# Performance work log

Measured on AMD Instinct MI355X. Metric: run time of the kernel, lower is better.

Reference implementation:

```python
import jax, jax.numpy as jnp
import numpy as np
from jax import lax

C = 256          # hidden_channels
K_ITERS = 3      # num_iterations

def _conv(x, w, b, stride=1, pad='SAME'):
    y = lax.conv_general_dilated(x, w, (stride, stride), pad,
                                 dimension_numbers=('NCHW', 'OIHW', 'NCHW'))
    return y + b[None, :, None, None]

def setup_inputs() -> dict:
    key = jax.random.key(0)
    ks = jax.random.split(key, 16)
    B, N, H, W = 1, 3, 384, 384
    def p(k, sh, scale=None):
        if scale is None:
            scale = 1.0 / np.sqrt(np.prod(sh[1:]))
        return jax.random.normal(k, sh, jnp.float32) * scale
    z = lambda: jnp.zeros((C,), jnp.float32)
    return {
        'frames': jax.random.normal(ks[0], (B, N, 3, H, W), jnp.float32),
        'backbone_w': p(ks[1], (C, 3, 8, 8)), 'backbone_b': z(),
        'W_intra': p(ks[2], (C, C), scale=1.0 / C),
        'W_inter': p(ks[3], (C, C), scale=1.0 / C),
        'gate_w': p(ks[4], (C, C, 1, 1)), 'gate_b': z(),
        'Wz': p(ks[5], (C, 2 * C, 3, 3)), 'bz': z(),
        'Wr': p(ks[6], (C, 2 * C, 3, 3)), 'br': z(),
        'Wh': p(ks[7], (C, 2 * C, 3, 3)), 'bh': z(),
        'ro_w1': p(ks[8], (C, 2 * C, 3, 3)), 'ro_b1': z(),
        'ro_w2': p(ks[9], (1, C, 3, 3)), 'ro_b2': jnp.zeros((1,), jnp.float32),
    }

def _forward(frames, backbone_w, backbone_b, W_intra, W_inter, gate_w, gate_b,
             Wz, bz, Wr, br, Wh, bh, ro_w1, ro_b1, ro_w2, ro_b2):
    B, N, _, H, W = frames.shape
    x = frames.reshape(B * N, 3, H, W)
    # backbone: stride-8 conv + ReLU -> node embeddings v (B*N, C, Hf, Wf)
    v = jax.nn.relu(_conv(x, backbone_w, backbone_b, stride=8, pad='VALID'))
    Hf, Wf = v.shape[2], v.shape[3]
    P = Hf * Wf
    v = v.reshape(B, N, C, Hf, Wf)
    h = v
    idx = jnp.arange(N)
    for _ in range(K_ITERS):
        hp = h.reshape(B, N, C, P).transpose(0, 1, 3, 2)      # (B,N,P,C)
        # inter attention e_ij = h_i W h_j^T over all ordered pairs
        t = jnp.einsum('bipc,cd->bipd', hp, W_inter)
        e = jnp.einsum('bipd,bjqd->bijpq', t, hp)              # (B,N,N,P,P)
        # intra (loop-edge) attention on the diagonal, own weight
        ti = jnp.einsum('bipc,cd->bipd', hp, W_intra)
        e_intra = jnp.einsum('bipd,biqd->bipq', ti, hp)        # (B,N,P,P)
        e = e.at[:, idx, idx].set(e_intra)
        attn = jax.nn.softmax(e, axis=-1)
        m = jnp.einsum('bijpq,bjqc->bijpc', attn, hp)          # msg j->i (B,N,N,P,C)
        m = m.transpose(0, 1, 2, 4, 3).reshape(B * N * N, C, Hf, Wf)
        # gated aggregation: sigmoid(1x1 conv) gate, sum over senders j
        g = jax.nn.sigmoid(_conv(m, gate_w, gate_b))
        magg = (g * m).reshape(B, N, N, C, Hf, Wf).sum(axis=2).reshape(B * N, C, Hf, Wf)
        # ConvGRU update
        hflat = h.reshape(B * N, C, Hf, Wf)
        mh = jnp.concatenate([magg, hflat], axis=1)
        zg = jax.nn.sigmoid(_conv(mh, Wz, bz))
        rg = jax.nn.sigmoid(_conv(mh, Wr, br))
        hc = jnp.tanh(_conv(jnp.concatenate([magg, rg * hflat], axis=1), Wh, bh))
        h = ((1.0 - zg) * hflat + zg * hc).reshape(B, N, C, Hf, Wf)
    # read-out on concat(h, v)
    cat = jnp.concatenate([h, v], axis=2).reshape(B * N, 2 * C, Hf, Wf)
    y = jax.nn.relu(_conv(cat, ro_w1, ro_b1))
    masks = _conv(y, ro_w2, ro_b2)
    return masks.reshape(B, N, 1, Hf, Wf)

def reference(frames, backbone_w, backbone_b, W_intra, W_inter, gate_w, gate_b,
              Wz, bz, Wr, br, Wh, bh, ro_w1, ro_b1, ro_w2, ro_b2):
    return _forward(frames, backbone_w, backbone_b, W_intra, W_inter, gate_w, gate_b,
                    Wz, bz, Wr, br, Wh, bh, ro_w1, ro_b1, ro_w2, ro_b2)
```

## Files before the change

### kernel.cpp

```cpp
#include <hip/hip_runtime.h>
#include <hip/hip_bf16.h>
#include <math.h>

#define PIX 2304
#define CCH 256
#define CP  589824
#define NCP 1769472
#define KC  4608
#define PADR 2512

typedef __hip_bfloat16 bf16;
typedef __attribute__((ext_vector_type(8))) short bf16x8;
typedef __attribute__((ext_vector_type(4))) float f32x4;

__device__ __forceinline__ float sigmoidf_(float x){ return 1.f/(1.f+__expf(-x)); }

__device__ __forceinline__ void gl_lds16(const bf16* g, bf16* lds){
    __builtin_amdgcn_global_load_lds(
        (const __attribute__((address_space(1))) void*)g,
        (__attribute__((address_space(3))) void*)lds, 16, 0, 0);
}
#define FENCE() asm volatile("" ::: "memory")

__device__ __forceinline__ float bperm_f(int srcLane, float v){
    return __int_as_float(__builtin_amdgcn_ds_bpermute(srcLane<<2, __float_as_int(v)));
}
__device__ __forceinline__ unsigned packbf(float lo, float hi){
    bf16 a = __float2bfloat16(lo), b = __float2bfloat16(hi);
    return (unsigned)(*(unsigned short*)&a) | ((unsigned)(*(unsigned short*)&b)<<16);
}

__global__ __launch_bounds__(512) void fattn_k(
    const bf16* __restrict__ T, const bf16* __restrict__ Ti,
    const bf16* __restrict__ Khp, const bf16* __restrict__ Vcp,
    bf16* __restrict__ Ob)
{
    __shared__ bf16 Ks[2][64*256];
    __shared__ bf16 Vs[2][256*64];
    __shared__ unsigned Ps[8][512];
    const int z = blockIdx.z, i = z/3, j = z%3;
    const bf16* Q  = ((i==j)? Ti : T) + (long)i*CP;
    const bf16* Kp = Khp + (long)j*CP;
    const bf16* Vp = Vcp + (long)j*CP;
    const int tid = threadIdx.x, l = tid & 63, w = tid >> 6;
    const int g = l>>4, m = l&15;
    const int q0 = blockIdx.x*128;

    bf16x8 qf[8];
    {
        const bf16* qr = Q + (long)(q0 + w*16 + m)*256 + g*8;
        #pragma unroll
        for (int ks=0; ks<8; ++ks) qf[ks] = *(const bf16x8*)(qr + ks*32);
    }
    f32x4 oacc[16];
    #pragma unroll
    for (int nf=0; nf<16; ++nf) oacc[nf] = (f32x4){0.f,0.f,0.f,0.f};
    float mrun = -3e38f;
    float lrun = 0.f;

    auto stage = [&](int buf, int t){
        const int kq = t*64;
        #pragma unroll
        for (int u=0; u<4; ++u){
            int idx = u*512 + tid;
            int rr = idx>>5, cc = idx&31;
            gl_lds16(Kp + (long)(kq+rr)*256 + ((cc ^ (rr&7))<<3),
                     &Ks[buf][(u*512 + (tid & ~63))*8]);
        }
        #pragma unroll
        for (int u=0; u<4; ++u){
            int idx = u*512 + tid;
            int rr = idx>>3, cc = idx&7;
            gl_lds16(Vp + (long)rr*2304 + kq + ((cc ^ (rr&7))<<3),
                     &Vs[buf][(u*512 + (tid & ~63))*8]);
        }
    };

    stage(0, 0);
    int cur = 0;
    char* pw = (char*)&Ps[w][0];
    for (int t=0; t<36; ++t){
        if (t+1 < 36){
            stage(cur^1, t+1);
            asm volatile("s_waitcnt vmcnt(8)" ::: "memory");
        } else {
            asm volatile("s_waitcnt vmcnt(0)" ::: "memory");
        }
        __builtin_amdgcn_s_barrier();
        FENCE();

        f32x4 sacc[4];
        #pragma unroll
        for (int nf=0; nf<4; ++nf) sacc[nf] = (f32x4){0.f,0.f,0.f,0.f};
        __builtin_amdgcn_s_setprio(1);
        #pragma unroll
        for (int ks=0; ks<8; ++ks){
            #pragma unroll
            for (int nf=0; nf<4; ++nf){
                int row = nf*16 + m;
                int phys = (ks*4 + g) ^ (row&7);
                bf16x8 kf = *(const bf16x8*)&Ks[cur][row*256 + phys*8];
                sacc[nf] = __builtin_amdgcn_mfma_f32_16x16x32_bf16(kf, qf[ks], sacc[nf], 0,0,0);
            }
        }
        __builtin_amdgcn_s_setprio(0);

        float pmax = -3e38f;
        #pragma unroll
        for (int nf=0; nf<4; ++nf)
            #pragma unroll
            for (int r=0; r<4; ++r) pmax = fmaxf(pmax, sacc[nf][r]);
        pmax = fmaxf(pmax, __shfl_xor(pmax, 16));
        pmax = fmaxf(pmax, __shfl_xor(pmax, 32));
        if (!__all(pmax - mrun <= 8.f)){
            float mn = fmaxf(mrun, pmax);
            float al = __expf(mrun - mn);
            mrun = mn;
            lrun *= al;
            float ar[4];
            #pragma unroll
            for (int r=0; r<4; ++r) ar[r] = bperm_f((l & 48) | (g*4 + r), al);
            #pragma unroll
            for (int nf=0; nf<16; ++nf)
                #pragma unroll
                for (int r=0; r<4; ++r) oacc[nf][r] *= ar[r];
        }
        float rs = 0.f;
        unsigned pk[4][2];
        #pragma unroll
        for (int nf=0; nf<4; ++nf){
            float p0 = __expf(sacc[nf][0] - mrun);
            float p1 = __expf(sacc[nf][1] - mrun);
            float p2 = __expf(sacc[nf][2] - mrun);
            float p3 = __expf(sacc[nf][3] - mrun);
            rs += (p0+p1) + (p2+p3);
            pk[nf][0] = packbf(p0, p1);
            pk[nf][1] = packbf(p2, p3);
        }
        rs += __shfl_xor(rs, 16);
        rs += __shfl_xor(rs, 32);
        lrun += rs;
        #pragma unroll
        for (int nf=0; nf<4; ++nf)
            #pragma unroll
            for (int s=0; s<2; ++s){
                int ba = m*128 + ((nf*32 + g*8 + s*4) ^ ((m&7)<<4));
                *(unsigned*)(pw + ba) = pk[nf][s];
            }
        asm volatile("s_waitcnt lgkmcnt(0)" ::: "memory");
        __builtin_amdgcn_sched_barrier(0);
        __builtin_amdgcn_s_setprio(1);
        #pragma unroll
        for (int ks2=0; ks2<2; ++ks2){
            bf16x8 pa = *(const bf16x8*)(pw + m*128 + ((ks2*64 + g*16) ^ ((m&7)<<4)));
            #pragma unroll
            for (int nf=0; nf<16; ++nf){
                int row = nf*16 + m;
                int phys = (ks2*4 + g) ^ (row&7);
                bf16x8 bv = *(const bf16x8*)&Vs[cur][row*64 + phys*8];
                oacc[nf] = __builtin_amdgcn_mfma_f32_16x16x32_bf16(pa, bv, oacc[nf], 0,0,0);
            }
        }
        __builtin_amdgcn_s_setprio(0);
        FENCE();
        __builtin_amdgcn_s_barrier();
        FENCE();
        cur ^= 1;
    }

    float linv = 1.f / lrun;
    float li[4];
    #pragma unroll
    for (int r=0; r<4; ++r) li[r] = bperm_f((l & 48) | (g*4 + r), linv);
    bf16* ob = Ob + (long)z*CP;
    const int prow0 = q0 + w*16 + g*4;
    #pragma unroll
    for (int nf=0; nf<16; ++nf){
        int c = nf*16 + m;
        #pragma unroll
        for (int r=0; r<4; ++r)
            ob[(long)(prow0+r)*256 + c] = __float2bfloat16(oacc[nf][r]*li[r]);
    }
}

template<int BN>
__global__ __launch_bounds__(256) void mgemm_k(
    const bf16* __restrict__ A0, const bf16* __restrict__ B, bf16* __restrict__ ob,
    int M, int lda, int ldb, int ldc,
    long bsB, long bsC, int nzJ, int Ksub)
{
    __shared__ bf16 As[2][128*64];
    __shared__ bf16 Bs[2][BN*64];
    const int jz = blockIdx.z % nzJ;
    const bf16* Ap = A0 + (long)blockIdx.x*128*lda;
    const bf16* Bp = B + jz*bsB + (long)blockIdx.y*BN*ldb;
    const int tid = threadIdx.x, l = tid & 63;
    const int wvu = tid & ~63;
    const int wr = tid>>7, wc = (tid>>6)&1;
    constexpr int NF = BN/32;
    f32x4 acc[4][NF];
    #pragma unroll
    for (int i=0;i<4;++i)
        #pragma unroll
        for (int j=0;j<NF;++j) acc[i][j] = (f32x4){0.f,0.f,0.f,0.f};

    auto stage = [&](int buf, int kb){
        #pragma unroll
        for (int u=0;u<4;++u){
            int idx = u*256 + tid;
            int row = idx>>3, g = (idx&7) ^ (row&7);
            gl_lds16(Ap + (long)row*lda + kb + g*8, &As[buf][(u*256+wvu)*8]);
        }
        #pragma unroll
        for (int u=0;u<BN/32;++u){
            int idx = u*256 + tid;
            int row = idx>>3, g = (idx&7) ^ (row&7);
            gl_lds16(Bp + (long)row*ldb + kb + g*8, &Bs[buf][(u*256+wvu)*8]);
        }
    };

    const int nk = Ksub >> 6;
    stage(0, 0);
    int cur = 0;
    for (int t=0; t<nk; ++t){
        if (t+1 < nk){
            stage(cur^1, (t+1)*64);
            if constexpr (BN==64) asm volatile("s_waitcnt vmcnt(6)" ::: "memory");
            else                  asm volatile("s_waitcnt vmcnt(8)" ::: "memory");
        } else {
            asm volatile("s_waitcnt vmcnt(0)" ::: "memory");
        }
        __builtin_amdgcn_s_barrier();
        FENCE();
        #pragma unroll
        for (int ks=0; ks<64; ks+=32){
            bf16x8 af[4], bfr[NF];
            #pragma unroll
            for (int i=0;i<4;++i){
                int row = wr*64 + i*16 + (l&15);
                af[i] = *(const bf16x8*)&As[cur][row*64 + ((((ks>>3)+(l>>4)) ^ (row&7))<<3)];
            }
            #pragma unroll
            for (int j=0;j<NF;++j){
                int row = wc*(BN/2) + j*16 + (l&15);
                bfr[j] = *(const bf16x8*)&Bs[cur][row*64 + ((((ks>>3)+(l>>4)) ^ (row&7))<<3)];
            }
            #pragma unroll
            for (int i=0;i<4;++i)
                #pragma unroll
                for (int j=0;j<NF;++j)
                    acc[i][j] = __builtin_amdgcn_mfma_f32_16x16x32_bf16(af[i], bfr[j], acc[i][j], 0,0,0);
        }
        FENCE();
        __builtin_amdgcn_s_barrier();
        FENCE();
        cur ^= 1;
    }

    const int mb = blockIdx.x*128 + wr*64, nb = blockIdx.y*BN + wc*(BN/2);
    #pragma unroll
    for (int i=0;i<4;++i)
        #pragma unroll
        for (int j=0;j<NF;++j){
            int gm0 = mb + i*16 + ((l>>4)<<2);
            int gn  = nb + j*16 + (l&15);
            #pragma unroll
            for (int r=0;r<4;++r)
                ob[jz*bsC + (long)(gm0+r)*ldc + gn] = __float2bfloat16(acc[i][j][r]);
        }
}

__global__ __launch_bounds__(256) void gatemm_k(
    const bf16* __restrict__ gatew, const bf16* __restrict__ Mb9,
    const float* __restrict__ gb, float* __restrict__ magg)
{
    __shared__ bf16 As[2][128*64];
    __shared__ bf16 Bs[2][64*64];
    const int tid = threadIdx.x, l = tid & 63, wvu = tid & ~63;
    const int wr = tid>>7, wc = (tid>>6)&1;
    const int i = blockIdx.z;
    const bf16* Ap = gatew + (long)blockIdx.x*128*256;
    const int nb0 = blockIdx.y*64;
    f32x4 msum[4][2];
    #pragma unroll
    for (int a=0;a<4;++a){ msum[a][0]=(f32x4){0,0,0,0}; msum[a][1]=(f32x4){0,0,0,0}; }

    for (int j=0; j<3; ++j){
        const bf16* Bp = Mb9 + (long)(i*3+j)*CP + (long)nb0*256;
        f32x4 acc[4][2];
        #pragma unroll
        for (int a=0;a<4;++a){ acc[a][0]=(f32x4){0,0,0,0}; acc[a][1]=(f32x4){0,0,0,0}; }
        auto stage = [&](int buf, int kb){
            #pragma unroll
            for (int u=0;u<4;++u){
                int idx = u*256 + tid;
                int row = idx>>3, g = (idx&7) ^ (row&7);
                gl_lds16(Ap + (long)row*256 + kb + g*8, &As[buf][(u*256+wvu)*8]);
            }
            #pragma unroll
            for (int u=0;u<2;++u){
                int idx = u*256 + tid;
                int row = idx>>3, g = (idx&7) ^ (row&7);
                gl_lds16(Bp + (long)row*256 + kb + g*8, &Bs[buf][(u*256+wvu)*8]);
            }
        };
        stage(0, 0);
        int cur = 0;
        for (int t=0; t<4; ++t){
            if (t+1 < 4){
                stage(cur^1, (t+1)*64);
                asm volatile("s_waitcnt vmcnt(6)" ::: "memory");
            } else {
                asm volatile("s_waitcnt vmcnt(0)" ::: "memory");
            }
            __builtin_amdgcn_s_barrier();
            FENCE();
            #pragma unroll
            for (int ks=0; ks<64; ks+=32){
                bf16x8 af[4], bfr[2];
                #pragma unroll
                for (int a=0;a<4;++a){
                    int row = wr*64 + a*16 + (l&15);
                    af[a] = *(const bf16x8*)&As[cur][row*64 + ((((ks>>3)+(l>>4)) ^ (row&7))<<3)];
                }
                #pragma unroll
                for (int b=0;b<2;++b){
                    int row = wc*32 + b*16 + (l&15);
                    bfr[b] = *(const bf16x8*)&Bs[cur][row*64 + ((((ks>>3)+(l>>4)) ^ (row&7))<<3)];
                }
                #pragma unroll
                for (int a=0;a<4;++a)
                    #pragma unroll
                    for (int b=0;b<2;++b)
                        acc[a][b] = __builtin_amdgcn_mfma_f32_16x16x32_bf16(af[a], bfr[b], acc[a][b], 0,0,0);
            }
            FENCE();
            __builtin_amdgcn_s_barrier();
            FENCE();
            cur ^= 1;
        }
        const bf16* mbz = Mb9 + (long)(i*3+j)*CP;
        const int mb = blockIdx.x*128 + wr*64;
        #pragma unroll
        for (int a=0;a<4;++a)
            #pragma unroll
            for (int b=0;b<2;++b){
                int gm0 = mb + a*16 + ((l>>4)<<2);
                int gn  = nb0 + wc*32 + b*16 + (l&15);
                #pragma unroll
                for (int r=0;r<4;++r){
                    int gm = gm0 + r;
                    float g = sigmoidf_(acc[a][b][r] + gb[gm]);
                    float mv = __bfloat162float(mbz[(long)gn*256 + gm]);
                    msum[a][b][r] += g*mv;
                }
            }
    }
    const int mb = blockIdx.x*128 + wr*64;
    #pragma unroll
    for (int a=0;a<4;++a)
        #pragma unroll
        for (int b=0;b<2;++b){
            int gm0 = mb + a*16 + ((l>>4)<<2);
            int gn  = nb0 + wc*32 + b*16 + (l&15);
            #pragma unroll
            for (int r=0;r<4;++r)
                magg[(long)i*CP + (long)(gm0+r)*PIX + gn] = msum[a][b][r];
        }
}

__global__ __launch_bounds__(256) void cgemm2_k(
    const bf16* __restrict__ inpad, const bf16* __restrict__ W,
    float* __restrict__ part, int N)
{
    __shared__ bf16 As[2][128*64];
    __shared__ bf16 Bs[2][128*64];
    const int tid = threadIdx.x, l = tid & 63, wvu = tid & ~63;
    const int wr = tid>>7, wc = (tid>>6)&1;
    const int bx = blockIdx.x, by = blockIdx.y, kc = blockIdx.z;
    const int img = bx/18, m0 = (bx - img*18)*128;
    const bf16* Ab = inpad + (long)img*PADR*512;
    const bf16* Bb = W + (long)by*128*KC;
    f32x4 acc[4][4];
    #pragma unroll
    for (int i=0;i<4;++i)
        #pragma unroll
        for (int j=0;j<4;++j) acc[i][j] = (f32x4){0.f,0.f,0.f,0.f};

    auto stageA = [&](int buf, int k0){
        int tap = k0 >> 9, ci0 = k0 & 511;
        int dy = tap/3, dx = tap - 3*dy;
        int shift = (dy-1)*50 + (dx-1);
        #pragma unroll
        for (int u=0;u<4;++u){
            int idx = u*256 + tid;
            int row = idx>>3;
            int om = m0 + row;
            int prow = om + 2*(om/48) + 51 + shift;
            int g = (idx&7) ^ (row&7);
            gl_lds16(Ab + (long)prow*512 + ci0 + g*8, &As[buf][(u*256+wvu)*8]);
        }
    };
    auto stageB = [&](int buf, int k0){
        #pragma unroll
        for (int u=0;u<4;++u){
            int idx = u*256 + tid;
            int row = idx>>3;
            int g = (idx&7) ^ (row&7);
            gl_lds16(Bb + (long)row*KC + k0 + g*8, &Bs[buf][(u*256+wvu)*8]);
        }
    };

    const int kbeg = kc*2304;
    stageA(0, kbeg); stageB(0, kbeg);
    int cur = 0;
    for (int t=0; t<36; ++t){
        if (t+1 < 36){
            stageA(cur^1, kbeg+(t+1)*64); stageB(cur^1, kbeg+(t+1)*64);
            asm volatile("s_waitcnt vmcnt(8)" ::: "memory");
        } else {
            asm volatile("s_waitcnt vmcnt(0)" ::: "memory");
        }
        __builtin_amdgcn_s_barrier();
        FENCE();
        #pragma unroll
        for (int ks=0; ks<64; ks+=32){
            bf16x8 af[4], bfr[4];
            #pragma unroll
            for (int i=0;i<4;++i){
                int row = wr*64 + i*16 + (l&15);
                af[i] = *(const bf16x8*)&As[cur][row*64 + ((((ks>>3)+(l>>4)) ^ (row&7))<<3)];
            }
            #pragma unroll
            for (int j=0;j<4;++j){
                int row = wc*64 + j*16 + (l&15);
                bfr[j] = *(const bf16x8*)&Bs[cur][row*64 + ((((ks>>3)+(l>>4)) ^ (row&7))<<3)];
            }
            #pragma unroll
            for (int i=0;i<4;++i)
                #pragma unroll
                for (int j=0;j<4;++j)
                    acc[i][j] = __builtin_amdgcn_mfma_f32_16x16x32_bf16(af[i], bfr[j], acc[i][j], 0,0,0);
        }
        FENCE();
        __builtin_amdgcn_s_barrier();
        FENCE();
        cur ^= 1;
    }

    float* pbase = part + (long)kc*N*6912 + (long)img*2304;
    #pragma unroll
    for (int i=0;i<4;++i)
        #pragma unroll
        for (int j=0;j<4;++j){
            int gm0 = m0 + wr*64 + i*16 + ((l>>4)<<2);
            int gn  = by*128 + wc*64 + j*16 + (l&15);
            *(f32x4*)&pbase[(long)gn*6912 + gm0] = acc[i][j];
        }
}

template<int ACT, int DUAL>
__global__ __launch_bounds__(256) void cred_k(const float* __restrict__ part,
        const float* __restrict__ b0, const float* __restrict__ b1,
        float* __restrict__ o0, float* __restrict__ o1,
        const float* __restrict__ hmul, int N)
{
    int id = blockIdx.x*256 + threadIdx.x;
    int c = id / 6912, g = id - c*6912;
    int img = g / 2304, p = g - img*2304;
    float v = part[id] + part[id + (long)N*6912];
    if (DUAL && c >= 256){
        int co = c - 256;
        long oidx = (long)img*CP + (long)co*PIX + p;
        o1[oidx] = sigmoidf_(v + b1[co]) * hmul[oidx];
    } else {
        float r = v + b0[c];
        if (ACT==1) r = sigmoidf_(r);
        else if (ACT==2) r = tanhf(r);
        else r = fmaxf(r, 0.f);
        o0[(long)img*CP + (long)c*PIX + p] = r;
    }
}

__global__ __launch_bounds__(256) void credh_k(const float* __restrict__ part,
        const float* __restrict__ bh, const float* __restrict__ zg,
        float* __restrict__ h)
{
    int id = blockIdx.x*256 + threadIdx.x;
    int c = id / 6912, g = id - c*6912;
    int img = g / 2304, p = g - img*2304;
    float v = part[id] + part[id + 256L*6912];
    float hcv = tanhf(v + bh[c]);
    long oidx = (long)img*CP + (long)c*PIX + p;
    float z = zg[oidx];
    h[oidx] = (1.f - z)*h[oidx] + z*hcv;
}

__global__ __launch_bounds__(256) void padtr_k(const float* __restrict__ src,
        bf16* __restrict__ dst, int cofs)
{
    __shared__ float tile[64][65];
    const int img = blockIdx.z, p0 = blockIdx.x*64, c0 = blockIdx.y*64;
    const int t = threadIdx.x, tx = t&63, tq = t>>6;
    const float* s = src + (long)img*CP;
    #pragma unroll
    for (int u=0;u<16;++u){
        int r = tq + u*4;
        tile[r][tx] = s[(long)(c0+r)*PIX + p0 + tx];
    }
    __syncthreads();
    bf16* d = dst + (long)img*PADR*512 + cofs + c0;
    #pragma unroll
    for (int u=0;u<16;++u){
        int pl = tq + u*4;
        int p = p0 + pl;
        int prow = p + 2*(p/48) + 51;
        d[(long)prow*512 + tx] = __float2bfloat16(tile[tx][pl]);
    }
}

__global__ __launch_bounds__(256) void convw_k(const float* __restrict__ src,
        bf16* __restrict__ dst, int total)
{
    int idx = blockIdx.x*256 + threadIdx.x;
    if (idx >= total) return;
    int co = idx / KC, r = idx - co*KC;
    int tap = r >> 9, ci = r & 511;
    dst[idx] = __float2bfloat16(src[(long)co*KC + ci*9 + tap]);
}

__global__ __launch_bounds__(256) void prep_h_k(const float* __restrict__ h,
        bf16* __restrict__ hcp, bf16* __restrict__ hp)
{
    __shared__ float tile[64][65];
    const int i = blockIdx.z, p0 = blockIdx.x*64, c0 = blockIdx.y*64;
    const int t = threadIdx.x, tx = t&63, tq = t>>6;
    const float* src = h + (long)i*CP;
    #pragma unroll
    for (int s=0;s<16;++s){
        int r = tq + s*4;
        float v = src[(long)(c0+r)*PIX + p0 + tx];
        tile[r][tx] = v;
        hcp[(long)i*CP + (long)(c0+r)*PIX + p0 + tx] = __float2bfloat16(v);
    }
    __syncthreads();
    #pragma unroll
    for (int s=0;s<16;++s){
        int r = tq + s*4;
        hp[(long)i*CP + (long)(p0+r)*256 + c0 + tx] = __float2bfloat16(tile[tx][r]);
    }
}

__global__ __launch_bounds__(256) void convert_w_k(const float* __restrict__ wint,
    const float* __restrict__ wintra, const float* __restrict__ gw, bf16* __restrict__ o)
{
    int t = blockIdx.x*256 + threadIdx.x;
    int d = t >> 8, c = t & 255;
    o[t]          = __float2bfloat16(wint[c*256 + d]);
    o[65536 + t]  = __float2bfloat16(wintra[c*256 + d]);
    o[131072 + t] = __float2bfloat16(gw[t]);
}

__global__ __launch_bounds__(256) void backbone_k(
    const float* __restrict__ frames, const float* __restrict__ W,
    const float* __restrict__ bias, float* __restrict__ v, float* __restrict__ h)
{
    __shared__ float wl[3*64*4];
    const int n = blockIdx.z, o0 = blockIdx.y * 4;
    const int p = blockIdx.x * 256 + threadIdx.x;
    const int y = p / 48, x = p % 48;
    for (int e = threadIdx.x; e < 768; e += 256) {
        int o_sel = e / 192, rem = e % 192, ci = rem / 64, k = rem % 64;
        wl[(ci*64 + k)*4 + o_sel] = W[((long)(o0 + o_sel)*3 + ci)*64 + k];
    }
    __syncthreads();
    float acc[4] = {0.f,0.f,0.f,0.f};
    for (int ci = 0; ci < 3; ++ci) {
        const float* src = frames + (((long)n*3 + ci)*384) * 384;
        #pragma unroll
        for (int k = 0; k < 64; ++k) {
            int ky = k >> 3, kx = k & 7;
            float iv = src[(8*y + ky)*384 + 8*x + kx];
            float4 w = ((const float4*)wl)[ci*64 + k];
            acc[0] += iv*w.x; acc[1] += iv*w.y; acc[2] += iv*w.z; acc[3] += iv*w.w;
        }
    }
    #pragma unroll
    for (int oo = 0; oo < 4; ++oo) {
        float r = fmaxf(acc[oo] + bias[o0 + oo], 0.f);
        long idx = ((long)n*CCH + o0 + oo)*PIX + p;
        v[idx] = r; h[idx] = r;
    }
}

__global__ __launch_bounds__(256) void maskpart_k(const float* __restrict__ yin,
        const float* __restrict__ W, float* __restrict__ part)
{
    __shared__ float wl[288];
    const int cb = blockIdx.y * 32;
    for (int e = threadIdx.x; e < 288; e += 256) wl[e] = W[cb*9 + e];
    __syncthreads();
    int id = blockIdx.x*256 + threadIdx.x;
    int n = id / PIX, p = id - n*PIX;
    int y = p / 48, x = p % 48;
    float acc = 0.f;
    for (int ci = 0; ci < 32; ++ci) {
        const float* src = yin + ((long)n*CCH + cb + ci)*PIX;
        #pragma unroll
        for (int dy = 0; dy < 3; ++dy) {
            int yy = y + dy - 1;
            #pragma unroll
            for (int dx = 0; dx < 3; ++dx) {
                int xx = x + dx - 1;
                float iv = (yy >= 0 && yy < 48 && xx >= 0 && xx < 48) ? src[yy*48 + xx] : 0.f;
                acc += iv * wl[ci*9 + dy*3 + dx];
            }
        }
    }
    part[(long)blockIdx.y*(3*PIX) + id] = acc;
}

__global__ __launch_bounds__(256) void maskred_k(const float* __restrict__ part,
        const float* __restrict__ bias, float* __restrict__ out)
{
    int id = blockIdx.x*256 + threadIdx.x;
    float acc = bias[0];
    #pragma unroll
    for (int s = 0; s < 8; ++s) acc += part[(long)s*(3*PIX) + id];
    out[id] = acc;
}

extern "C" void kernel_launch(void* const* d_in, const int* in_sizes, int n_in,
                              void* d_out, int out_size, void* d_ws, size_t ws_size,
                              hipStream_t stream)
{
    const float* frames     = (const float*)d_in[0];
    const float* backbone_w = (const float*)d_in[1];
    const float* backbone_b = (const float*)d_in[2];
    const float* W_intra    = (const float*)d_in[3];
    const float* W_inter    = (const float*)d_in[4];
    const float* gate_w     = (const float*)d_in[5];
    const float* gate_b     = (const float*)d_in[6];
    const float* Wz         = (const float*)d_in[7];
    const float* bz         = (const float*)d_in[8];
    const float* Wr         = (const float*)d_in[9];
    const float* br         = (const float*)d_in[10];
    const float* Wh         = (const float*)d_in[11];
    const float* bh         = (const float*)d_in[12];
    const float* ro_w1      = (const float*)d_in[13];
    const float* ro_b1      = (const float*)d_in[14];
    const float* ro_w2      = (const float*)d_in[15];
    const float* ro_b2      = (const float*)d_in[16];
    float* out = (float*)d_out;
    float* ws  = (float*)d_ws;

    float* h    = ws + 0L*NCP;
    float* v    = ws + 1L*NCP;
    float* magg = ws + 2L*NCP;
    float* zg   = ws + 3L*NCP;
    float* rg   = ws + 4L*NCP;
    float* rhg  = ws + 5L*NCP;
    float* hcmb = ws + 6L*NCP;
    float* S    = ws + 7L*NCP;

    float* Mb9f   = S;
    float* hp16f  = S + 7962624;
    float* hcp16f = hp16f + 884736;
    float* t16f   = hcp16f + 884736;
    float* ti16f  = t16f + 884736;
    float* wbase  = S + 11501568;
    bf16* Wint_t   = (bf16*)wbase;
    bf16* Wintra_t = Wint_t + 65536;
    bf16* gatew16  = Wint_t + 131072;
    bf16* cw16     = (bf16*)(wbase + 98304);
    bf16* inpad    = (bf16*)(wbase + 98304 + 2359296);
    float* maskp   = wbase + 98304 + 2359296 + 1929216;

    bf16* Mb9    = (bf16*)Mb9f;
    bf16* hp16   = (bf16*)hp16f;
    bf16* hcp16  = (bf16*)hcp16f;
    bf16* t16    = (bf16*)t16f;
    bf16* ti16   = (bf16*)ti16f;
    float* cpart = Mb9f;

    dim3 b256(256);

    hipMemsetAsync(inpad, 0, 3858432*sizeof(bf16), stream);
    backbone_k<<<dim3(9,64,3), b256, 0, stream>>>(frames, backbone_w, backbone_b, v, h);
    convert_w_k<<<dim3(256), b256, 0, stream>>>(W_inter, W_intra, gate_w, Wint_t);
    convw_k<<<dim3(4608), b256, 0, stream>>>(Wz, cw16, 256*KC);
    convw_k<<<dim3(4608), b256, 0, stream>>>(Wr, cw16 + 256L*KC, 256*KC);
    convw_k<<<dim3(4608), b256, 0, stream>>>(Wh, cw16 + 512L*KC, 256*KC);
    convw_k<<<dim3(4608), b256, 0, stream>>>(ro_w1, cw16 + 768L*KC, 256*KC);

    for (int it = 0; it < 3; ++it) {
        prep_h_k<<<dim3(36,4,3), b256, 0, stream>>>(h, hcp16, hp16);
        mgemm_k<64><<<dim3(54,4,2), b256, 0, stream>>>(hp16, Wint_t, t16,
            6912, 256,256,256, 65536L, 1769472L, 2, 256);
        fattn_k<<<dim3(18,1,9), dim3(512), 0, stream>>>(t16, ti16, hp16, hcp16, Mb9);
        gatemm_k<<<dim3(2,36,3), b256, 0, stream>>>(gatew16, Mb9, gate_b, magg);
        padtr_k<<<dim3(36,4,3), b256, 0, stream>>>(magg, inpad, 0);
        padtr_k<<<dim3(36,4,3), b256, 0, stream>>>(h,    inpad, 256);
        cgemm2_k<<<dim3(54,4,2), b256, 0, stream>>>(inpad, cw16, cpart, 512);
        cred_k<1,1><<<dim3(13824), b256, 0, stream>>>(cpart, bz, br, zg, rhg, h, 512);
        padtr_k<<<dim3(36,4,3), b256, 0, stream>>>(rhg, inpad, 256);
        cgemm2_k<<<dim3(54,2,2), b256, 0, stream>>>(inpad, cw16 + 512L*KC, cpart, 256);
        credh_k<<<dim3(6912), b256, 0, stream>>>(cpart, bh, zg, h);
    }

    padtr_k<<<dim3(36,4,3), b256, 0, stream>>>(h, inpad, 0);
    padtr_k<<<dim3(36,4,3), b256, 0, stream>>>(v, inpad, 256);
    cgemm2_k<<<dim3(54,2,2), b256, 0, stream>>>(inpad, cw16 + 768L*KC, cpart, 256);
    cred_k<3,0><<<dim3(6912), b256, 0, stream>>>(cpart, ro_b1, nullptr, zg, nullptr, nullptr, 256);
    maskpart_k<<<dim3(27,8), b256, 0, stream>>>(zg, ro_w2, maskp);
    maskred_k<<<dim3(27), b256, 0, stream>>>(maskp, ro_b2, out);
}
```

Baseline: 904.2 us.

## Fuse transpose/pad staging into gate GEMM and GRU reduction epilogues

The gate GEMM now transposes its aggregated message through LDS and writes bf16 directly into the padded conv input, replacing the fp32 magg buffer and a separate padtr pass. The z/r reduction writes rg*h straight into the padded input. The h update now also emits the bf16 copies (hcp, hp) and the padded h used by the next iteration, so the per-iteration prep_h and padtr launches are dropped. This removes several full-tensor fp32 round trips and kernel launches per GRU iteration, at the cost of extra LDS use and more stores inside the fused kernels.

Result: faster. 866.2 us (-4.2%).

```diff
diff --git a/kernel.cpp b/kernel.cpp
--- a/kernel.cpp
+++ b/kernel.cpp
@@ -272,10 +272,11 @@
 
 __global__ __launch_bounds__(256) void gatemm_k(
     const bf16* __restrict__ gatew, const bf16* __restrict__ Mb9,
-    const float* __restrict__ gb, float* __restrict__ magg)
+    const float* __restrict__ gb, bf16* __restrict__ inpad)
 {
     __shared__ bf16 As[2][128*64];
     __shared__ bf16 Bs[2][64*64];
+    __shared__ bf16 Ts[64*136];
     const int tid = threadIdx.x, l = tid & 63, wvu = tid & ~63;
     const int wr = tid>>7, wc = (tid>>6)&1;
     const int i = blockIdx.z;
@@ -356,17 +357,26 @@
                 }
             }
     }
-    const int mb = blockIdx.x*128 + wr*64;
+    __syncthreads();
+    const int mbl = wr*64;
     #pragma unroll
     for (int a=0;a<4;++a)
         #pragma unroll
         for (int b=0;b<2;++b){
-            int gm0 = mb + a*16 + ((l>>4)<<2);
-            int gn  = nb0 + wc*32 + b*16 + (l&15);
+            int cl0 = mbl + a*16 + ((l>>4)<<2);
+            int pl  = wc*32 + b*16 + (l&15);
             #pragma unroll
             for (int r=0;r<4;++r)
-                magg[(long)i*CP + (long)(gm0+r)*PIX + gn] = msum[a][b][r];
-        }
+                Ts[pl*136 + cl0 + r] = __float2bfloat16(msum[a][b][r]);
+        }
+    __syncthreads();
+    const int pl = tid >> 2, seg = tid & 3;
+    int p = nb0 + pl;
+    int prow = p + 2*(p/48) + 51;
+    bf16* dst = inpad + (long)i*PADR*512 + (long)prow*512 + blockIdx.x*128 + seg*32;
+    #pragma unroll
+    for (int k2=0; k2<4; ++k2)
+        *(uint4*)(dst + k2*8) = *(const uint4*)&Ts[pl*136 + seg*32 + k2*8];
 }
 
 __global__ __launch_bounds__(256) void cgemm2_k(
@@ -459,41 +469,74 @@
         }
 }
 
-template<int ACT, int DUAL>
-__global__ __launch_bounds__(256) void cred_k(const float* __restrict__ part,
-        const float* __restrict__ b0, const float* __restrict__ b1,
-        float* __restrict__ o0, float* __restrict__ o1,
-        const float* __restrict__ hmul, int N)
-{
-    int id = blockIdx.x*256 + threadIdx.x;
-    int c = id / 6912, g = id - c*6912;
-    int img = g / 2304, p = g - img*2304;
-    float v = part[id] + part[id + (long)N*6912];
-    if (DUAL && c >= 256){
-        int co = c - 256;
-        long oidx = (long)img*CP + (long)co*PIX + p;
-        o1[oidx] = sigmoidf_(v + b1[co]) * hmul[oidx];
-    } else {
-        float r = v + b0[c];
-        if (ACT==1) r = sigmoidf_(r);
-        else if (ACT==2) r = tanhf(r);
-        else r = fmaxf(r, 0.f);
-        o0[(long)img*CP + (long)c*PIX + p] = r;
-    }
-}
-
-__global__ __launch_bounds__(256) void credh_k(const float* __restrict__ part,
+__global__ __launch_bounds__(256) void credzr_k(const float* __restrict__ part,
+        const float* __restrict__ bz, const float* __restrict__ br,
+        const float* __restrict__ h, float* __restrict__ zg, bf16* __restrict__ inpad)
+{
+    __shared__ float tz[64][65];
+    const int img = blockIdx.z, p0 = blockIdx.x*64, c0 = blockIdx.y*64;
+    const int t = threadIdx.x, tx = t&63, tq = t>>6;
+    #pragma unroll
+    for (int u=0;u<16;++u){
+        int cl = tq + u*4, c = c0 + cl;
+        long pz = (long)c*6912 + (long)img*2304 + p0 + tx;
+        float vz = part[pz] + part[pz + 512L*6912];
+        long pr = (long)(c+256)*6912 + (long)img*2304 + p0 + tx;
+        float vr = part[pr] + part[pr + 512L*6912];
+        long hidx = (long)img*CP + (long)c*PIX + p0 + tx;
+        float hv = h[hidx];
+        zg[hidx] = sigmoidf_(vz + bz[c]);
+        tz[cl][tx] = sigmoidf_(vr + br[c]) * hv;
+    }
+    __syncthreads();
+    #pragma unroll
+    for (int u=0;u<16;++u){
+        int pl = tq + u*4, p = p0 + pl;
+        int prow = p + 2*(p/48) + 51;
+        inpad[(long)img*PADR*512 + (long)prow*512 + 256 + c0 + tx] = __float2bfloat16(tz[tx][pl]);
+    }
+}
+
+__global__ __launch_bounds__(256) void credht_k(const float* __restrict__ part,
         const float* __restrict__ bh, const float* __restrict__ zg,
-        float* __restrict__ h)
+        float* __restrict__ h, bf16* __restrict__ hcp, bf16* __restrict__ hp,
+        bf16* __restrict__ inpad)
+{
+    __shared__ float th[64][65];
+    const int img = blockIdx.z, p0 = blockIdx.x*64, c0 = blockIdx.y*64;
+    const int t = threadIdx.x, tx = t&63, tq = t>>6;
+    #pragma unroll
+    for (int u=0;u<16;++u){
+        int cl = tq + u*4, c = c0 + cl;
+        long pidx = (long)c*6912 + (long)img*2304 + p0 + tx;
+        float vv = part[pidx] + part[pidx + 256L*6912];
+        float hc = tanhf(vv + bh[c]);
+        long hidx = (long)img*CP + (long)c*PIX + p0 + tx;
+        float zv = zg[hidx];
+        float hn = (1.f - zv)*h[hidx] + zv*hc;
+        h[hidx] = hn;
+        hcp[hidx] = __float2bfloat16(hn);
+        th[cl][tx] = hn;
+    }
+    __syncthreads();
+    #pragma unroll
+    for (int u=0;u<16;++u){
+        int pl = tq + u*4, p = p0 + pl;
+        float val = th[tx][pl];
+        hp[(long)img*CP + (long)p*256 + c0 + tx] = __float2bfloat16(val);
+        int prow = p + 2*(p/48) + 51;
+        inpad[(long)img*PADR*512 + (long)prow*512 + 256 + c0 + tx] = __float2bfloat16(val);
+    }
+}
+
+__global__ __launch_bounds__(256) void credro_k(const float* __restrict__ part,
+        const float* __restrict__ b0, float* __restrict__ o0)
 {
     int id = blockIdx.x*256 + threadIdx.x;
     int c = id / 6912, g = id - c*6912;
     int img = g / 2304, p = g - img*2304;
     float v = part[id] + part[id + 256L*6912];
-    float hcv = tanhf(v + bh[c]);
-    long oidx = (long)img*CP + (long)c*PIX + p;
-    float z = zg[oidx];
-    h[oidx] = (1.f - z)*h[oidx] + z*hcv;
+    o0[(long)img*CP + (long)c*PIX + p] = fmaxf(v + b0[c], 0.f);
 }
 
 __global__ __launch_bounds__(256) void padtr_k(const float* __restrict__ src,
@@ -502,11 +545,10 @@
     __shared__ float tile[64][65];
     const int img = blockIdx.z, p0 = blockIdx.x*64, c0 = blockIdx.y*64;
     const int t = threadIdx.x, tx = t&63, tq = t>>6;
-    const float* s = src + (long)img*CP;
     #pragma unroll
     for (int u=0;u<16;++u){
         int r = tq + u*4;
-        tile[r][tx] = s[(long)(c0+r)*PIX + p0 + tx];
+        tile[r][tx] = src[(long)img*CP + (long)(c0+r)*PIX + p0 + tx];
     }
     __syncthreads();
     bf16* d = dst + (long)img*PADR*512 + cofs + c0;
@@ -535,11 +577,10 @@
     __shared__ float tile[64][65];
     const int i = blockIdx.z, p0 = blockIdx.x*64, c0 = blockIdx.y*64;
     const int t = threadIdx.x, tx = t&63, tq = t>>6;
-    const float* src = h + (long)i*CP;
     #pragma unroll
     for (int s=0;s<16;++s){
         int r = tq + s*4;
-        float v = src[(long)(c0+r)*PIX + p0 + tx];
+        float v = h[(long)i*CP + (long)(c0+r)*PIX + p0 + tx];
         tile[r][tx] = v;
         hcp[(long)i*CP + (long)(c0+r)*PIX + p0 + tx] = __float2bfloat16(v);
     }
@@ -693,25 +734,24 @@
     convw_k<<<dim3(4608), b256, 0, stream>>>(Wh, cw16 + 512L*KC, 256*KC);
     convw_k<<<dim3(4608), b256, 0, stream>>>(ro_w1, cw16 + 768L*KC, 256*KC);
 
+    prep_h_k<<<dim3(36,4,3), b256, 0, stream>>>(h, hcp16, hp16);
+    padtr_k<<<dim3(36,4,3), b256, 0, stream>>>(h, inpad, 256);
+
     for (int it = 0; it < 3; ++it) {
-        prep_h_k<<<dim3(36,4,3), b256, 0, stream>>>(h, hcp16, hp16);
         mgemm_k<64><<<dim3(54,4,2), b256, 0, stream>>>(hp16, Wint_t, t16,
             6912, 256,256,256, 65536L, 1769472L, 2, 256);
         fattn_k<<<dim3(18,1,9), dim3(512), 0, stream>>>(t16, ti16, hp16, hcp16, Mb9);
-        gatemm_k<<<dim3(2,36,3), b256, 0, stream>>>(gatew16, Mb9, gate_b, magg);
-        padtr_k<<<dim3(36,4,3), b256, 0, stream>>>(magg, inpad, 0);
-        padtr_k<<<dim3(36,4,3), b256, 0, stream>>>(h,    inpad, 256);
+        gatemm_k<<<dim3(2,36,3), b256, 0, stream>>>(gatew16, Mb9, gate_b, inpad);
         cgemm2_k<<<dim3(54,4,2), b256, 0, stream>>>(inpad, cw16, cpart, 512);
-        cred_k<1,1><<<dim3(13824), b256, 0, stream>>>(cpart, bz, br, zg, rhg, h, 512);
-        padtr_k<<<dim3(36,4,3), b256, 0, stream>>>(rhg, inpad, 256);
+        credzr_k<<<dim3(36,4,3), b256, 0, stream>>>(cpart, bz, br, h, zg, inpad);
         cgemm2_k<<<dim3(54,2,2), b256, 0, stream>>>(inpad, cw16 + 512L*KC, cpart, 256);
-        credh_k<<<dim3(6912), b256, 0, stream>>>(cpart, bh, zg, h);
+        credht_k<<<dim3(36,4,3), b256, 0, stream>>>(cpart, bh, zg, h, hcp16, hp16, inpad);
     }
 
     padtr_k<<<dim3(36,4,3), b256, 0, stream>>>(h, inpad, 0);
     padtr_k<<<dim3(36,4,3), b256, 0, stream>>>(v, inpad, 256);
     cgemm2_k<<<dim3(54,2,2), b256, 0, stream>>>(inpad, cw16 + 768L*KC, cpart, 256);
-    cred_k<3,0><<<dim3(6912), b256, 0, stream>>>(cpart, ro_b1, nullptr, zg, nullptr, nullptr, 256);
+    credro_k<<<dim3(6912), b256, 0, stream>>>(cpart, ro_b1, zg);
     maskpart_k<<<dim3(27,8), b256, 0, stream>>>(zg, ro_w2, maskp);
     maskred_k<<<dim3(27), b256, 0, stream>>>(maskp, ro_b2, out);
 }
```
